# Kernel optimization log

Hardware: AMD Instinct MI355X
Metric: run time of the kernel (lower is better)

## Reference

```python
import math
import jax, jax.numpy as jnp
import numpy as np

L, F, K = 3, 128, 20          # layers, hidden size, rbf size
CUTOFF = 5.0
B, NPER, EPER = 4, 4096, 49152  # graphs, nodes/graph, edges/graph
NVOC = 119                    # len(ase.data.atomic_numbers)
PNAMES = ['atom_emb','pot_W','pot_b','init_W1','init_b1','init_W2','init_b2','vec_w',
          'filt_W','filt_b','msg_W1','msg_b1','msg_W2','msg_b2','U_W','V_W',
          'upd_W1','upd_b1','upd_W2','upd_b2']


def _painn(atom_xyz, cell, nodes, atom_edges, edges_displacement, V_flat, E_flat, p):
    N = B * NPER
    pos = atom_xyz.reshape(N, 3)
    # edge_offset = cumsum(num_nodes) ; all graphs have NPER nodes
    off = (jnp.arange(B, dtype=atom_edges.dtype) * NPER)[:, None, None]
    edges = (atom_edges + off).reshape(B * EPER, 2)
    # calc_distance with periodic cell offsets
    disp = jnp.einsum('bec,bcd->bed', edges_displacement, cell).reshape(B * EPER, 3)
    send, recv = edges[:, 0], edges[:, 1]
    diff = pos[recv] - (pos[send] + disp)                       # [E,3]
    dist = jnp.sqrt(jnp.sum(diff * diff, axis=1, keepdims=True))  # [E,1]
    # sinc RBF expansion
    n_range = jnp.arange(1, K + 1, dtype=jnp.float32)
    edge_state = jnp.sin(dist * n_range * (math.pi / CUTOFF)) / dist  # [E,K]
    # init scalar features: Embedding(Z) || Linear(V) -> MLP
    s_atom = p['atom_emb'][nodes.reshape(N)]                    # [N,F]
    s_pot = V_flat @ p['pot_W'].T + p['pot_b']                  # [N,F]
    h = jnp.concatenate([s_atom, s_pot], axis=-1)
    s = jax.nn.silu(h @ p['init_W1'].T + p['init_b1']) @ p['init_W2'].T + p['init_b2']  # [N,F]
    # init vector features: no-bias Linear(1->F) on E field
    v = E_flat[:, :, None] * p['vec_w']                         # [N,3,F]
    cut = jnp.where(dist < CUTOFF, 0.5 * (jnp.cos(math.pi * dist / CUTOFF) + 1.0), 0.0)  # [E,1]
    dirn = diff / jnp.maximum(dist, 1e-12)                      # [E,3]
    s_list, v_list = [], []
    for l in range(L):
        # --- PaiNNInteraction ---
        fw = (edge_state @ p['filt_W'][l].T + p['filt_b'][l]) * cut                # [E,3F]
        so = jax.nn.silu(s @ p['msg_W1'][l].T + p['msg_b1'][l]) @ p['msg_W2'][l].T + p['msg_b2'][l]  # [N,3F]
        fo = fw * so[send]                                                          # [E,3F]
        g_sv, g_ev, g_ns = jnp.split(fo, 3, axis=1)
        msg_s = s[send] * g_ns                                                      # [E,F]
        msg_v = v[send] * g_sv[:, None, :] + g_ev[:, None, :] * dirn[:, :, None]    # [E,3,F]
        s = s + jax.ops.segment_sum(msg_s, recv, num_segments=N)
        v = v + jax.ops.segment_sum(msg_v, recv, num_segments=N)
        # --- PaiNNUpdate ---
        Uv = v @ p['U_W'][l].T                                                      # [N,3,F]
        Vv = v @ p['V_W'][l].T                                                      # [N,3,F]
        Vn = jnp.sqrt(jnp.sum(Vv * Vv, axis=1))                                     # [N,F]
        m = jnp.concatenate([s, Vn], axis=1)
        m = jax.nn.silu(m @ p['upd_W1'][l].T + p['upd_b1'][l]) @ p['upd_W2'][l].T + p['upd_b2'][l]
        a_ss, a_sv, a_vv = jnp.split(m, 3, axis=1)
        s = s + a_ss + a_sv * jnp.sum(Uv * Vv, axis=1)
        v = v + a_vv[:, None, :] * Uv
        s_list.append(s)
        v_list.append(v)
    # pack trajectory: [L,N,1,F] scalar || [L,N,3,F] vector -> [L,N,4,F]
    return jnp.concatenate([jnp.stack(s_list)[:, :, None, :], jnp.stack(v_list)], axis=2)


def setup_inputs() -> dict:
    key = jax.random.key(0)
    ks = iter(jax.random.split(key, 48))
    def nrm(shape, scale=0.05):
        return jax.random.normal(next(ks), shape, dtype=jnp.float32) * scale
    atom_xyz = jax.random.uniform(next(ks), (B, NPER, 3), dtype=jnp.float32) * 30.0
    cell = jnp.tile(jnp.eye(3, dtype=jnp.float32)[None] * 30.0, (B, 1, 1))
    nodes = jax.random.randint(next(ks), (B, NPER), 0, NVOC)
    e0 = jax.random.randint(next(ks), (B, EPER), 0, NPER)
    delta = jax.random.randint(next(ks), (B, EPER), 1, NPER)
    e1 = (e0 + delta) % NPER  # sender != receiver -> no zero-distance edges
    atom_edges = jnp.stack([e0, e1], axis=-1)
    edges_displacement = jax.random.randint(next(ks), (B, EPER, 3), -1, 2).astype(jnp.float32)
    V_flat = nrm((B * NPER, 1), 1.0)
    E_flat = nrm((B * NPER, 3), 1.0)
    params = dict(
        atom_emb=nrm((NVOC, F), 1.0),
        pot_W=nrm((F, 1)), pot_b=nrm((F,)),
        init_W1=nrm((F, 2 * F)), init_b1=nrm((F,)),
        init_W2=nrm((F, F)), init_b2=nrm((F,)),
        vec_w=nrm((F,)),
        filt_W=nrm((L, 3 * F, K)), filt_b=nrm((L, 3 * F)),
        msg_W1=nrm((L, F, F)), msg_b1=nrm((L, F)),
        msg_W2=nrm((L, 3 * F, F)), msg_b2=nrm((L, 3 * F)),
        U_W=nrm((L, F, F)), V_W=nrm((L, F, F)),
        upd_W1=nrm((L, F, 2 * F)), upd_b1=nrm((L, F)),
        upd_W2=nrm((L, 3 * F, F)), upd_b2=nrm((L, 3 * F)),
    )
    return dict(atom_xyz=atom_xyz, cell=cell, nodes=nodes, atom_edges=atom_edges,
                edges_displacement=edges_displacement, V_flat=V_flat, E_flat=E_flat, **params)


def reference(atom_xyz, cell, nodes, atom_edges, edges_displacement, V_flat, E_flat,
              atom_emb, pot_W, pot_b, init_W1, init_b1, init_W2, init_b2, vec_w,
              filt_W, filt_b, msg_W1, msg_b1, msg_W2, msg_b2, U_W, V_W,
              upd_W1, upd_b1, upd_W2, upd_b2):
    p = dict(zip(PNAMES, (atom_emb, pot_W, pot_b, init_W1, init_b1, init_W2, init_b2, vec_w,
                          filt_W, filt_b, msg_W1, msg_b1, msg_W2, msg_b2, U_W, V_W,
                          upd_W1, upd_b1, upd_W2, upd_b2)))
    return _painn(atom_xyz, cell, nodes, atom_edges, edges_displacement, V_flat, E_flat, p)
```

## Files before the change

### kernel.cpp

```cpp
#include <hip/hip_runtime.h>
#include <math.h>

#define NPER  4096
#define NTOT  16384
#define EPER  49152
#define ETOT  196608
#define FD    128
#define F3    384
#define KR    20
#define PI_F  3.14159265358979f

typedef unsigned short u16;
typedef __attribute__((ext_vector_type(8))) short s16x8;
typedef __attribute__((ext_vector_type(4))) float f32x4;
typedef _Float16 h16x2 __attribute__((ext_vector_type(2)));
typedef _Float16 h16x4 __attribute__((ext_vector_type(4)));
typedef _Float16 h16x8 __attribute__((ext_vector_type(8)));

#if defined(__has_builtin)
#if __has_builtin(__builtin_amdgcn_fdot2)
#define FDOT2(a,b,c) __builtin_amdgcn_fdot2((a),(b),(c),false)
#endif
#endif
#ifndef FDOT2
#define FDOT2(a,b,c) ((float)(a)[0]*(float)(b)[0] + (float)(a)[1]*(float)(b)[1] + (c))
#endif

__device__ __forceinline__ float silu_f(float x){ return x / (1.0f + __expf(-x)); }
__device__ __forceinline__ u16 f2b(float x){
    unsigned u = __float_as_uint(x);
    u = u + 0x7FFFu + ((u >> 16) & 1u);
    return (u16)(u >> 16);
}
__device__ __forceinline__ float b2f(u16 h){ return __uint_as_float(((unsigned)h) << 16); }

struct __align__(16) EdgeRec {
    float4 ed;
    h16x8  es0;
    h16x8  es1;
    h16x4  es2;
    h16x4  pad;
};

__global__ __launch_bounds__(256) void edge_kernel(
    const float* __restrict__ xyz, const float* __restrict__ cell,
    const int* __restrict__ aedges, const float* __restrict__ edisp,
    int* __restrict__ sendb, int* __restrict__ recvb,
    EdgeRec* __restrict__ erec, int* __restrict__ counts)
{
    int e = blockIdx.x * blockDim.x + threadIdx.x;
    if (e >= ETOT) return;
    int b = e / EPER;
    int s = aedges[(size_t)e*2+0] + b*NPER;
    int r = aedges[(size_t)e*2+1] + b*NPER;
    const float* cb = cell + b*9;
    float c0 = edisp[(size_t)e*3+0], c1 = edisp[(size_t)e*3+1], c2 = edisp[(size_t)e*3+2];
    float diff[3];
    #pragma unroll
    for (int d=0; d<3; ++d) {
        float disp = c0*cb[d] + c1*cb[3+d] + c2*cb[6+d];
        diff[d] = xyz[(size_t)r*3+d] - (xyz[(size_t)s*3+d] + disp);
    }
    float dist = sqrtf(diff[0]*diff[0]+diff[1]*diff[1]+diff[2]*diff[2]);
    float cut = (dist < 5.0f) ? 0.5f*(__cosf(PI_F*dist*0.2f)+1.0f) : 0.0f;
    float invg = 1.0f/fmaxf(dist,1e-12f);
    EdgeRec rec;
    rec.ed = make_float4(diff[0]*invg, diff[1]*invg, diff[2]*invg, cut);
    float theta = dist*(PI_F*0.2f);
    float s1 = __sinf(theta), cth = __cosf(theta);
    float scale = cut / dist;
    float twoc = 2.f*cth;
    float sm1 = 0.f, sk = s1;
    _Float16 esv[20];
    #pragma unroll
    for (int k=0;k<20;++k){
        esv[k] = (_Float16)(sk*scale);
        float nx = twoc*sk - sm1;
        sm1 = sk; sk = nx;
    }
    union { h16x8 v; _Float16 h[8]; } u0, u1;
    union { h16x4 v; _Float16 h[4]; } u2;
    #pragma unroll
    for (int i=0;i<8;++i){ u0.h[i]=esv[i]; u1.h[i]=esv[8+i]; }
    #pragma unroll
    for (int i=0;i<4;++i) u2.h[i]=esv[16+i];
    rec.es0=u0.v; rec.es1=u1.v; rec.es2=u2.v;
    rec.pad = (h16x4)((_Float16)0);
    erec[e] = rec;
    sendb[e]=s; recvb[e]=r;
    atomicAdd(&counts[r],1);
}

__global__ __launch_bounds__(1024) void scan_kernel(const int* __restrict__ counts,
                                                    int* __restrict__ row_off)
{
    __shared__ int sdata[1024];
    int t = threadIdx.x;
    int base = t * 16;
    int local[16];
    int s = 0;
    #pragma unroll
    for (int i=0;i<16;++i){ local[i]=s; s += counts[base+i]; }
    sdata[t] = s;
    __syncthreads();
    for (int off=1; off<1024; off<<=1) {
        int val = (t>=off) ? sdata[t-off] : 0;
        __syncthreads();
        sdata[t] += val;
        __syncthreads();
    }
    int chunk_off = (t==0) ? 0 : sdata[t-1];
    #pragma unroll
    for (int i=0;i<16;++i) row_off[base+i] = chunk_off + local[i];
    if (t==1023) row_off[NTOT] = sdata[1023];
}

__global__ __launch_bounds__(256) void fill_kernel(
    const int* __restrict__ recvb, const int* __restrict__ sendb,
    const EdgeRec* __restrict__ erec,
    const int* __restrict__ row_off, int* __restrict__ cursor,
    int* __restrict__ sd_csr, EdgeRec* __restrict__ erec_csr)
{
    int e = blockIdx.x * blockDim.x + threadIdx.x;
    if (e >= ETOT) return;
    int r = recvb[e];
    int slot = atomicAdd(&cursor[r], 1);
    int pos = row_off[r] + slot;
    sd_csr[pos] = sendb[e];
    erec_csr[pos] = erec[e];
}

__global__ __launch_bounds__(256) void wconv_kernel(
    const float* __restrict__ w0, const float* __restrict__ w1,
    const float* __restrict__ w2, const float* __restrict__ w3,
    const float* __restrict__ w4, const float* __restrict__ w5,
    const float* __restrict__ w6, const float* __restrict__ w7,
    u16* __restrict__ dst)
{
    int t = blockIdx.x*256 + threadIdx.x;
    if (t >= 589824) return;
    const float* src; int off; int d = t;
    if      (t < 32768)  { src=w0; off=t; }
    else if (t < 49152)  { src=w1; off=t-32768; }
    else if (t < 98304)  { src=w2; off=t-49152; }
    else if (t < 245760) { src=w3; off=t-98304; }
    else if (t < 294912) { int o=t-245760; int l=o>>14; int r=o&16383; src=w4; off=o;
                           d = 245760 + l*32768 + r; }
    else if (t < 344064) { int o=t-294912; int l=o>>14; int r=o&16383; src=w5; off=o;
                           d = 245760 + l*32768 + 16384 + r; }
    else if (t < 442368) { src=w6; off=t-344064; }
    else                 { src=w7; off=t-442368; }
    dst[d] = f2b(src[off]);
}

__global__ __launch_bounds__(256) void wfilt_kernel(const float* __restrict__ fW,
                                                    _Float16* __restrict__ dst)
{
    int t = blockIdx.x*256 + threadIdx.x;
    if (t < 3*F3*KR) dst[t] = (_Float16)fW[t];
}

__global__ __launch_bounds__(256) void hbuild_kernel(const int* __restrict__ nodes,
    const float* __restrict__ atom_emb, const float* __restrict__ V_flat,
    const float* __restrict__ pot_W, const float* __restrict__ pot_b,
    u16* __restrict__ h)
{
    int t = blockIdx.x * blockDim.x + threadIdx.x;
    int n = t >> 8, k = t & 255;
    float val;
    if (k < FD) val = atom_emb[(size_t)nodes[n]*FD + k];
    else { int f = k - FD; val = V_flat[n]*pot_W[f] + pot_b[f]; }
    h[t] = f2b(val);
}

__global__ __launch_bounds__(256) void v0_kernel(const float* __restrict__ E_flat,
    const float* __restrict__ vec_w, float* __restrict__ v0, u16* __restrict__ vq)
{
    int t = blockIdx.x * blockDim.x + threadIdx.x;
    int n = t / F3, r = t - n*F3;
    int c = r >> 7, f = r & 127;
    float val = E_flat[(size_t)n*3 + c] * vec_w[f];
    v0[t] = val;
    vq[((size_t)n*FD + f)*4 + c] = f2b(val);
}

template<int ACT>
__global__ __launch_bounds__(256) void bgemm_kernel(
    const u16* __restrict__ A, int lda,
    const u16* __restrict__ W, int Kdim,
    const float* __restrict__ bias,
    float* __restrict__ C, int ldc,
    u16* __restrict__ Cb, int ldcb,
    u16* __restrict__ Cq, int qoff)
{
    const int tid  = threadIdx.x;
    const int wave = tid >> 6, lane = tid & 63;
    const int q = lane >> 4, im = lane & 15;
    const int row0 = blockIdx.y*64 + wave*16;
    const int col0 = blockIdx.x*64;
    f32x4 acc[4];
    #pragma unroll
    for (int n=0;n<4;++n) acc[n] = (f32x4){0.f,0.f,0.f,0.f};
    const u16* Ap = A + (size_t)(row0+im)*lda + q*8;
    const u16* Wp = W + (size_t)(col0+im)*Kdim + q*8;
    for (int k0 = 0; k0 < Kdim; k0 += 32) {
        s16x8 af = *(const s16x8*)(Ap + k0);
        #pragma unroll
        for (int n=0;n<4;++n) {
            s16x8 bf = *(const s16x8*)(Wp + (size_t)n*16*Kdim + k0);
            acc[n] = __builtin_amdgcn_mfma_f32_16x16x32_bf16(af, bf, acc[n], 0, 0, 0);
        }
    }
    #pragma unroll
    for (int n=0;n<4;++n) {
        int col = col0 + n*16 + im;
        float bv = bias ? bias[col] : 0.f;
        #pragma unroll
        for (int r=0;r<4;++r) {
            int row = row0 + q*4 + r;
            float v = acc[n][r] + bv;
            if (ACT) v = silu_f(v);
            if (C)  C[(size_t)row*ldc + col] = v;
            if (Cb) Cb[(size_t)row*ldcb + col] = f2b(v);
            if (Cq) Cq[((size_t)row*FD + (col & 127))*4 + (col >> 7) + qoff] = f2b(v);
        }
    }
}

__global__ __launch_bounds__(256) void uvdot_kernel(
    const u16* __restrict__ A,
    const u16* __restrict__ W,
    float* __restrict__ Uv,
    float* __restrict__ dotb,
    u16* __restrict__ mbuf)
{
    const int tid  = threadIdx.x;
    const int wave = tid >> 6, lane = tid & 63;
    const int q = lane >> 4, im = lane & 15;
    const int row0 = blockIdx.x*64 + wave*16;
    const int node = (row0 >> 2) + q;
    const u16* Ap = A + (size_t)(row0+im)*FD + q*8;
    s16x8 af[4];
    #pragma unroll
    for (int k=0;k<4;++k) af[k] = *(const s16x8*)(Ap + k*32);
    #pragma unroll
    for (int j=0;j<8;++j) {
        f32x4 aU = (f32x4){0.f,0.f,0.f,0.f};
        f32x4 aV = (f32x4){0.f,0.f,0.f,0.f};
        const u16* WpU = W + (size_t)(j*16+im)*FD + q*8;
        const u16* WpV = WpU + (size_t)128*FD;
        #pragma unroll
        for (int k=0;k<4;++k) {
            s16x8 bU = *(const s16x8*)(WpU + k*32);
            s16x8 bV = *(const s16x8*)(WpV + k*32);
            aU = __builtin_amdgcn_mfma_f32_16x16x32_bf16(af[k], bU, aU, 0, 0, 0);
            aV = __builtin_amdgcn_mfma_f32_16x16x32_bf16(af[k], bV, aV, 0, 0, 0);
        }
        int fcol = j*16 + im;
        float u0=aU[0], u1=aU[1], u2=aU[2];
        float w0=aV[0], w1=aV[1], w2=aV[2];
        dotb[(size_t)node*FD + fcol] = u0*w0 + u1*w1 + u2*w2;
        mbuf[(size_t)node*256 + FD + fcol] = f2b(sqrtf(w0*w0 + w1*w1 + w2*w2));
        size_t ub = ((size_t)node*4)*FD + fcol;
        Uv[ub]      = u0;
        Uv[ub+FD]   = u1;
        Uv[ub+2*FD] = u2;
    }
}

__global__ __launch_bounds__(256) void updepi_kernel(
    const u16* __restrict__ A,
    const u16* __restrict__ W,
    const float* __restrict__ bias,
    const float* __restrict__ s_mid, const float* __restrict__ dotb,
    const float* __restrict__ v_mid, const float* __restrict__ Uv,
    float* __restrict__ outp, u16* __restrict__ s_bf,
    u16* __restrict__ sq, u16* __restrict__ vq)
{
    const int tid  = threadIdx.x;
    const int wave = tid >> 6, lane = tid & 63;
    const int q = lane >> 4, im = lane & 15;
    const int rowgrp = wave >> 1, jhalf = wave & 1;
    const int row0 = blockIdx.x*32 + rowgrp*16;
    const u16* Ap = A + (size_t)(row0+im)*FD + q*8;

    for (int j = jhalf*4; j < jhalf*4+4; ++j) {
        f32x4 acc[3];
        #pragma unroll
        for (int g=0; g<3; ++g) acc[g] = (f32x4){0.f,0.f,0.f,0.f};
        const u16* Wp0 = W + (size_t)(j*16 + im)*FD + q*8;
        #pragma unroll
        for (int k0 = 0; k0 < FD; k0 += 32) {
            s16x8 af = *(const s16x8*)(Ap + k0);
            #pragma unroll
            for (int g=0; g<3; ++g) {
                s16x8 bf = *(const s16x8*)(Wp0 + (size_t)g*FD*FD + k0);
                acc[g] = __builtin_amdgcn_mfma_f32_16x16x32_bf16(af, bf, acc[g], 0, 0, 0);
            }
        }
        int fcol = j*16 + im;
        float b_ss = bias[fcol], b_sv = bias[FD+fcol], b_vv = bias[2*FD+fcol];
        #pragma unroll
        for (int r=0;r<4;++r) {
            int row = row0 + q*4 + r;
            float a_ss = acc[0][r] + b_ss;
            float a_sv = acc[1][r] + b_sv;
            float a_vv = acc[2][r] + b_vv;
            size_t t = (size_t)row*FD + fcol;
            float sval = s_mid[t] + a_ss + a_sv*dotb[t];
            outp[(size_t)row*512 + fcol] = sval;
            s_bf[t] = f2b(sval);
            sq[t*4 + 3] = f2b(sval);
            ushort4 pack;
            #pragma unroll
            for (int c=0;c<3;++c) {
                size_t vi = ((size_t)row*3 + c)*FD + fcol;
                float vval = v_mid[vi] + a_vv*Uv[((size_t)row*4 + c)*FD + fcol];
                outp[(size_t)row*512 + (1+c)*FD + fcol] = vval;
                ((u16*)&pack)[c] = f2b(vval);
            }
            ((u16*)&pack)[3] = 0;
            *(ushort4*)(vq + t*4) = pack;
        }
    }
}

__device__ __forceinline__ void edge_step(
    const EdgeRec& er, ushort4 s4, ushort4 v4,
    const h16x2* wp,
    float b0, float b1, float b2,
    float& acc_s, float& av0, float& av1, float& av2)
{
    union { h16x8 v; h16x2 p[4]; } e0, e1;
    union { h16x4 v; h16x2 p[2]; } e2;
    e0.v = er.es0; e1.v = er.es1; e2.v = er.es2;
    h16x2 ep[10] = {e0.p[0],e0.p[1],e0.p[2],e0.p[3],
                    e1.p[0],e1.p[1],e1.p[2],e1.p[3],
                    e2.p[0],e2.p[1]};
    float4 ed = er.ed;
    float d0=0.f, d1=0.f, d2=0.f;
    #pragma unroll
    for (int j=0;j<10;++j){
        d0 = FDOT2(ep[j], wp[j],    d0);
        d1 = FDOT2(ep[j], wp[10+j], d1);
        d2 = FDOT2(ep[j], wp[20+j], d2);
    }
    float g_sv = d0 + b0*ed.w;
    float g_ev = d1 + b1*ed.w;
    float g_ns = d2 + b2*ed.w;
    float fo_sv = g_sv * b2f(s4.x);
    float fo_ev = g_ev * b2f(s4.y);
    float fo_ns = g_ns * b2f(s4.z);
    acc_s += b2f(s4.w) * fo_ns;
    av0 += b2f(v4.x)*fo_sv + fo_ev*ed.x;
    av1 += b2f(v4.y)*fo_sv + fo_ev*ed.y;
    av2 += b2f(v4.z)*fo_sv + fo_ev*ed.z;
}

__global__ __launch_bounds__(256) __attribute__((amdgpu_waves_per_eu(4,8)))
void agg_kernel(
    const float* __restrict__ s_prev_f, int s_ldaf,
    const float* __restrict__ v_prev_f, int v_nstrf,
    const ushort4* __restrict__ sq, const ushort4* __restrict__ vq,
    const EdgeRec* __restrict__ erec_csr,
    const int* __restrict__ sd_csr, const int* __restrict__ row_off,
    const _Float16* __restrict__ wf, const float* __restrict__ fb,
    float* __restrict__ s_mid, float* __restrict__ v_mid,
    u16* __restrict__ vmid4_bf, u16* __restrict__ mbuf)
{
    const int f   = threadIdx.x & 127;
    const int sub = threadIdx.x >> 7;
    h16x2 wp[30];
    #pragma unroll
    for (int rsel=0; rsel<3; ++rsel){
        const h16x4* rp = (const h16x4*)(wf + (size_t)(rsel*FD + f)*KR);
        #pragma unroll
        for (int i=0;i<5;++i){
            union { h16x4 v; h16x2 p[2]; } t; t.v = rp[i];
            wp[rsel*10+2*i]   = t.p[0];
            wp[rsel*10+2*i+1] = t.p[1];
        }
    }
    const float b0 = fb[f], b1 = fb[FD+f], b2 = fb[2*FD+f];

    const int n = blockIdx.x*2 + sub;
    const int beg = __builtin_amdgcn_readfirstlane(row_off[n]);
    const int end = __builtin_amdgcn_readfirstlane(row_off[n+1]);
    float acc_s=0.f, av0=0.f, av1=0.f, av2=0.f;

    int i0 = (beg   < end) ? beg   : 0;
    int i1 = (beg+1 < end) ? beg+1 : i0;
    int sd0 = __builtin_amdgcn_readfirstlane(sd_csr[i0]);
    int sd1 = __builtin_amdgcn_readfirstlane(sd_csr[i1]);
    ushort4 sA = sq[(size_t)sd0*FD + f];
    ushort4 vA = vq[(size_t)sd0*FD + f];
    ushort4 sB = sq[(size_t)sd1*FD + f];
    ushort4 vB = vq[(size_t)sd1*FD + f];
    EdgeRec r0 = erec_csr[i0];
    EdgeRec r1 = erec_csr[i1];

    for (int idx = beg; idx + 2 <= end; idx += 2) {
        int j0 = (idx+2 < end) ? idx+2 : 0;
        int j1 = (idx+3 < end) ? idx+3 : j0;
        int nsd0 = __builtin_amdgcn_readfirstlane(sd_csr[j0]);
        int nsd1 = __builtin_amdgcn_readfirstlane(sd_csr[j1]);
        ushort4 nsA = sq[(size_t)nsd0*FD + f];
        ushort4 nvA = vq[(size_t)nsd0*FD + f];
        ushort4 nsB = sq[(size_t)nsd1*FD + f];
        ushort4 nvB = vq[(size_t)nsd1*FD + f];
        EdgeRec nr0 = erec_csr[j0];
        EdgeRec nr1 = erec_csr[j1];

        edge_step(r0, sA, vA, wp, b0,b1,b2, acc_s, av0, av1, av2);
        edge_step(r1, sB, vB, wp, b0,b1,b2, acc_s, av0, av1, av2);

        sA=nsA; vA=nvA; sB=nsB; vB=nvB; r0=nr0; r1=nr1;
    }
    if (((end - beg) & 1) && beg < end) {
        edge_step(r0, sA, vA, wp, b0,b1,b2, acc_s, av0, av1, av2);
    }

    float smv = s_prev_f[(size_t)n*s_ldaf+f] + acc_s;
    s_mid[(size_t)n*FD+f] = smv;
    mbuf[(size_t)n*256+f] = f2b(smv);
    const float* vp = v_prev_f + (size_t)n*v_nstrf;
    float o0 = vp[f]+av0, o1 = vp[FD+f]+av1, o2 = vp[2*FD+f]+av2;
    size_t vo = (size_t)n*F3;
    v_mid[vo+f]=o0;        v_mid[vo+FD+f]=o1;        v_mid[vo+2*FD+f]=o2;
    size_t v4 = (size_t)n*512;
    vmid4_bf[v4+f]=f2b(o0); vmid4_bf[v4+FD+f]=f2b(o1); vmid4_bf[v4+2*FD+f]=f2b(o2);
}

extern "C" void kernel_launch(void* const* d_in, const int* in_sizes, int n_in,
                              void* d_out, int out_size, void* d_ws, size_t ws_size,
                              hipStream_t stream)
{
    (void)in_sizes; (void)n_in; (void)out_size; (void)ws_size;
    const float* atom_xyz = (const float*)d_in[0];
    const float* cell     = (const float*)d_in[1];
    const int*   nodes    = (const int*)d_in[2];
    const int*   aedges   = (const int*)d_in[3];
    const float* edisp    = (const float*)d_in[4];
    const float* V_flat   = (const float*)d_in[5];
    const float* E_flat   = (const float*)d_in[6];
    const float* atom_emb = (const float*)d_in[7];
    const float* pot_W    = (const float*)d_in[8];
    const float* pot_b    = (const float*)d_in[9];
    const float* init_W1  = (const float*)d_in[10];
    const float* init_b1  = (const float*)d_in[11];
    const float* init_W2  = (const float*)d_in[12];
    const float* init_b2  = (const float*)d_in[13];
    const float* vec_w    = (const float*)d_in[14];
    const float* filt_W   = (const float*)d_in[15];
    const float* filt_b   = (const float*)d_in[16];
    const float* msg_W1   = (const float*)d_in[17];
    const float* msg_b1   = (const float*)d_in[18];
    const float* msg_W2   = (const float*)d_in[19];
    const float* msg_b2   = (const float*)d_in[20];
    const float* U_W      = (const float*)d_in[21];
    const float* V_W      = (const float*)d_in[22];
    const float* upd_W1   = (const float*)d_in[23];
    const float* upd_b1   = (const float*)d_in[24];
    const float* upd_W2   = (const float*)d_in[25];
    const float* upd_b2   = (const float*)d_in[26];

    float* out = (float*)d_out;
    char* base = (char*)d_ws;
    size_t o = 0;
    auto alloc = [&](size_t bytes)->char* { char* r = base + o; o += (bytes + 255) & ~(size_t)255; return r; };

    float* s0     = (float*)alloc((size_t)NTOT*FD*4);
    float* v0     = (float*)alloc((size_t)NTOT*F3*4);
    float* s_mid  = (float*)alloc((size_t)NTOT*FD*4);
    float* v_mid  = (float*)alloc((size_t)NTOT*F3*4);
    float* Uv4    = (float*)alloc((size_t)NTOT*4*FD*4);
    float* dotb   = (float*)alloc((size_t)NTOT*FD*4);
    EdgeRec* erec     = (EdgeRec*)alloc((size_t)ETOT*sizeof(EdgeRec));
    EdgeRec* erec_csr = (EdgeRec*)alloc((size_t)ETOT*sizeof(EdgeRec));
    u16* h_bf     = (u16*)alloc((size_t)NTOT*256*2);
    u16* s_bf     = (u16*)alloc((size_t)NTOT*FD*2);
    u16* sq       = (u16*)alloc((size_t)NTOT*FD*4*2);
    u16* vq       = (u16*)alloc((size_t)NTOT*FD*4*2);
    u16* hid_bf   = (u16*)alloc((size_t)NTOT*FD*2);
    u16* vmid4_bf = (u16*)alloc((size_t)NTOT*4*FD*2);
    u16* wts      = (u16*)alloc((size_t)589824*2);
    _Float16* wf16 = (_Float16*)alloc((size_t)3*F3*KR*2);
    int* sendb    = (int*)alloc((size_t)ETOT*4);
    int* recvb    = (int*)alloc((size_t)ETOT*4);
    int* sd_csr   = (int*)alloc((size_t)ETOT*4);
    int* row_off  = (int*)alloc((size_t)(NTOT+1)*4);
    int* counts   = (int*)alloc((size_t)NTOT*4);
    int* cursor   = (int*)alloc((size_t)NTOT*4);

    hipMemsetAsync(counts, 0, NTOT*sizeof(int), stream);
    hipMemsetAsync(cursor, 0, NTOT*sizeof(int), stream);
    hipMemsetAsync(vmid4_bf, 0, (size_t)NTOT*4*FD*2, stream);

    edge_kernel<<<ETOT/256, 256, 0, stream>>>(atom_xyz, cell, aedges, edisp,
        sendb, recvb, erec, counts);
    scan_kernel<<<1, 1024, 0, stream>>>(counts, row_off);
    fill_kernel<<<ETOT/256, 256, 0, stream>>>(recvb, sendb, erec,
        row_off, cursor, sd_csr, erec_csr);
    wconv_kernel<<<(589824+255)/256, 256, 0, stream>>>(
        init_W1, init_W2, msg_W1, msg_W2, U_W, V_W, upd_W1, upd_W2, wts);
    wfilt_kernel<<<(3*F3*KR+255)/256, 256, 0, stream>>>(filt_W, wf16);

    const u16* w_init1 = wts + 0;
    const u16* w_init2 = wts + 32768;
    const u16* w_msg1  = wts + 49152;
    const u16* w_msg2  = wts + 98304;
    const u16* w_UV    = wts + 245760;
    const u16* w_upd1  = wts + 344064;
    const u16* w_upd2  = wts + 442368;

    hbuild_kernel<<<NTOT*256/256, 256, 0, stream>>>(nodes, atom_emb, V_flat, pot_W, pot_b, h_bf);
    bgemm_kernel<1><<<dim3(FD/64, NTOT/64), 256, 0, stream>>>(
        h_bf, 256, w_init1, 256, init_b1, (float*)nullptr, 0, hid_bf, FD, (u16*)nullptr, 0);
    bgemm_kernel<0><<<dim3(FD/64, NTOT/64), 256, 0, stream>>>(
        hid_bf, FD, w_init2, FD, init_b2, s0, FD, s_bf, FD, sq, 3);
    v0_kernel<<<NTOT*F3/256, 256, 0, stream>>>(E_flat, vec_w, v0, vq);

    const float* s_prev_f = s0;  int s_ldaf  = FD;
    const float* v_prev_f = v0;  int v_nstrf = 3*FD;
    for (int l = 0; l < 3; ++l) {
        bgemm_kernel<1><<<dim3(FD/64, NTOT/64), 256, 0, stream>>>(
            s_bf, FD, w_msg1 + (size_t)l*16384, FD, msg_b1 + (size_t)l*FD,
            (float*)nullptr, 0, hid_bf, FD, (u16*)nullptr, 0);
        bgemm_kernel<0><<<dim3(F3/64, NTOT/64), 256, 0, stream>>>(
            hid_bf, FD, w_msg2 + (size_t)l*49152, FD, msg_b2 + (size_t)l*F3,
            (float*)nullptr, 0, (u16*)nullptr, 0, sq, 0);
        agg_kernel<<<NTOT/2, 256, 0, stream>>>(s_prev_f, s_ldaf, v_prev_f, v_nstrf,
            (const ushort4*)sq, (const ushort4*)vq, erec_csr, sd_csr, row_off,
            wf16 + (size_t)l*F3*KR, filt_b + (size_t)l*F3, s_mid, v_mid, vmid4_bf, h_bf);
        uvdot_kernel<<<NTOT*4/64, 256, 0, stream>>>(
            vmid4_bf, w_UV + (size_t)l*32768, Uv4, dotb, h_bf);
        bgemm_kernel<1><<<dim3(FD/64, NTOT/64), 256, 0, stream>>>(
            h_bf, 256, w_upd1 + (size_t)l*32768, 256, upd_b1 + (size_t)l*FD,
            (float*)nullptr, 0, hid_bf, FD, (u16*)nullptr, 0);
        float* outp = out + (size_t)l*NTOT*512;
        updepi_kernel<<<NTOT/32, 256, 0, stream>>>(
            hid_bf, w_upd2 + (size_t)l*49152, upd_b2 + (size_t)l*F3,
            s_mid, dotb, v_mid, Uv4, outp, s_bf, sq, vq);
        s_prev_f = outp;        s_ldaf  = 512;
        v_prev_f = outp + FD;   v_nstrf = 512;
    }
}
```

Baseline: 795.6 us.

## Fuse two-layer message and update MLPs into single kernels via LDS hidden tile

Replaces the pair of bgemm launches for the message MLP, and the bgemm plus updepi launches for the update MLP, with single 512-thread kernels. Each kernel computes the first GEMM with SiLU into an XOR-swizzled shared-memory hidden tile, then runs the second GEMM from LDS. This removes the hid_bf global round-trip and two launches per layer. In exchange, blocks are larger, LDS use per block is higher, and weights are read directly from global per wave, which may lower occupancy.

```diff
diff --git a/kernel.cpp b/kernel.cpp
--- a/kernel.cpp
+++ b/kernel.cpp
@@ -227,85 +227,156 @@
     }
 }
 
-__global__ __launch_bounds__(256) void uvdot_kernel(
+#define HID_OFF(row, col2b) ((unsigned)((row)*256 + (col2b)*2) ^ ((unsigned)((row)&7) << 4))
+
+__global__ __launch_bounds__(512) void msgmlp_kernel(
     const u16* __restrict__ A,
-    const u16* __restrict__ W,
-    float* __restrict__ Uv,
-    float* __restrict__ dotb,
-    u16* __restrict__ mbuf)
-{
-    const int tid  = threadIdx.x;
+    const u16* __restrict__ W1,
+    const float* __restrict__ b1,
+    const u16* __restrict__ W2,
+    const float* __restrict__ b2,
+    u16* __restrict__ sq)
+{
+    __shared__ u16 hid[64*FD];
+    const int tid = threadIdx.x;
     const int wave = tid >> 6, lane = tid & 63;
     const int q = lane >> 4, im = lane & 15;
-    const int row0 = blockIdx.x*64 + wave*16;
-    const int node = (row0 >> 2) + q;
-    const u16* Ap = A + (size_t)(row0+im)*FD + q*8;
+    const int rw = (wave >> 1) * 16;
+    const int ch = wave & 1;
+    const int row0 = blockIdx.x * 64;
+    {
+        f32x4 acc[4];
+        #pragma unroll
+        for (int n=0;n<4;++n) acc[n] = (f32x4){0.f,0.f,0.f,0.f};
+        const u16* Ap = A + (size_t)(row0+rw+im)*FD + q*8;
+        #pragma unroll
+        for (int k0=0;k0<FD;k0+=32) {
+            s16x8 af = *(const s16x8*)(Ap + k0);
+            #pragma unroll
+            for (int n=0;n<4;++n) {
+                s16x8 bf = *(const s16x8*)(W1 + (size_t)(ch*64+n*16+im)*FD + k0 + q*8);
+                acc[n] = __builtin_amdgcn_mfma_f32_16x16x32_bf16(af, bf, acc[n], 0, 0, 0);
+            }
+        }
+        #pragma unroll
+        for (int n=0;n<4;++n) {
+            int col = ch*64 + n*16 + im;
+            float bv = b1[col];
+            #pragma unroll
+            for (int r=0;r<4;++r) {
+                int row = rw + q*4 + r;
+                *(u16*)((char*)hid + HID_OFF(row, col)) = f2b(silu_f(acc[n][r]+bv));
+            }
+        }
+    }
+    __syncthreads();
     s16x8 af[4];
-    #pragma unroll
-    for (int k=0;k<4;++k) af[k] = *(const s16x8*)(Ap + k*32);
-    #pragma unroll
-    for (int j=0;j<8;++j) {
-        f32x4 aU = (f32x4){0.f,0.f,0.f,0.f};
-        f32x4 aV = (f32x4){0.f,0.f,0.f,0.f};
-        const u16* WpU = W + (size_t)(j*16+im)*FD + q*8;
-        const u16* WpV = WpU + (size_t)128*FD;
+    {
+        int row = rw + im;
+        #pragma unroll
+        for (int k=0;k<4;++k)
+            af[k] = *(const s16x8*)((char*)hid + HID_OFF(row, k*32+q*8));
+    }
+    #pragma unroll
+    for (int jj=0;jj<4;++jj) {
+        int j = ch*4 + jj;
+        f32x4 a2[3];
+        #pragma unroll
+        for (int g=0;g<3;++g) a2[g] = (f32x4){0.f,0.f,0.f,0.f};
         #pragma unroll
         for (int k=0;k<4;++k) {
-            s16x8 bU = *(const s16x8*)(WpU + k*32);
-            s16x8 bV = *(const s16x8*)(WpV + k*32);
-            aU = __builtin_amdgcn_mfma_f32_16x16x32_bf16(af[k], bU, aU, 0, 0, 0);
-            aV = __builtin_amdgcn_mfma_f32_16x16x32_bf16(af[k], bV, aV, 0, 0, 0);
+            #pragma unroll
+            for (int g=0;g<3;++g) {
+                s16x8 bf = *(const s16x8*)(W2 + (size_t)(g*128 + j*16 + im)*FD + k*32 + q*8);
+                a2[g] = __builtin_amdgcn_mfma_f32_16x16x32_bf16(af[k], bf, a2[g], 0, 0, 0);
+            }
         }
         int fcol = j*16 + im;
-        float u0=aU[0], u1=aU[1], u2=aU[2];
-        float w0=aV[0], w1=aV[1], w2=aV[2];
-        dotb[(size_t)node*FD + fcol] = u0*w0 + u1*w1 + u2*w2;
-        mbuf[(size_t)node*256 + FD + fcol] = f2b(sqrtf(w0*w0 + w1*w1 + w2*w2));
-        size_t ub = ((size_t)node*4)*FD + fcol;
-        Uv[ub]      = u0;
-        Uv[ub+FD]   = u1;
-        Uv[ub+2*FD] = u2;
-    }
-}
-
-__global__ __launch_bounds__(256) void updepi_kernel(
+        float c0 = b2[fcol], c1 = b2[FD+fcol], c2 = b2[2*FD+fcol];
+        #pragma unroll
+        for (int r=0;r<4;++r) {
+            int row = row0 + rw + q*4 + r;
+            size_t t4 = ((size_t)row*FD + fcol)*4;
+            unsigned pk = (unsigned)f2b(a2[0][r]+c0) | ((unsigned)f2b(a2[1][r]+c1) << 16);
+            *(unsigned*)(sq + t4) = pk;
+            sq[t4+2] = f2b(a2[2][r]+c2);
+        }
+    }
+}
+
+__global__ __launch_bounds__(512) void updmlp_kernel(
     const u16* __restrict__ A,
-    const u16* __restrict__ W,
-    const float* __restrict__ bias,
+    const u16* __restrict__ W1,
+    const float* __restrict__ b1,
+    const u16* __restrict__ W2,
+    const float* __restrict__ b2,
     const float* __restrict__ s_mid, const float* __restrict__ dotb,
     const float* __restrict__ v_mid, const float* __restrict__ Uv,
     float* __restrict__ outp, u16* __restrict__ s_bf,
     u16* __restrict__ sq, u16* __restrict__ vq)
 {
-    const int tid  = threadIdx.x;
+    __shared__ u16 hid[64*FD];
+    const int tid = threadIdx.x;
     const int wave = tid >> 6, lane = tid & 63;
     const int q = lane >> 4, im = lane & 15;
-    const int rowgrp = wave >> 1, jhalf = wave & 1;
-    const int row0 = blockIdx.x*32 + rowgrp*16;
-    const u16* Ap = A + (size_t)(row0+im)*FD + q*8;
-
-    for (int j = jhalf*4; j < jhalf*4+4; ++j) {
-        f32x4 acc[3];
-        #pragma unroll
-        for (int g=0; g<3; ++g) acc[g] = (f32x4){0.f,0.f,0.f,0.f};
-        const u16* Wp0 = W + (size_t)(j*16 + im)*FD + q*8;
-        #pragma unroll
-        for (int k0 = 0; k0 < FD; k0 += 32) {
+    const int rw = (wave >> 1) * 16;
+    const int ch = wave & 1;
+    const int row0 = blockIdx.x * 64;
+    {
+        f32x4 acc[4];
+        #pragma unroll
+        for (int n=0;n<4;++n) acc[n] = (f32x4){0.f,0.f,0.f,0.f};
+        const u16* Ap = A + (size_t)(row0+rw+im)*256 + q*8;
+        #pragma unroll
+        for (int k0=0;k0<256;k0+=32) {
             s16x8 af = *(const s16x8*)(Ap + k0);
             #pragma unroll
-            for (int g=0; g<3; ++g) {
-                s16x8 bf = *(const s16x8*)(Wp0 + (size_t)g*FD*FD + k0);
-                acc[g] = __builtin_amdgcn_mfma_f32_16x16x32_bf16(af, bf, acc[g], 0, 0, 0);
+            for (int n=0;n<4;++n) {
+                s16x8 bf = *(const s16x8*)(W1 + (size_t)(ch*64+n*16+im)*256 + k0 + q*8);
+                acc[n] = __builtin_amdgcn_mfma_f32_16x16x32_bf16(af, bf, acc[n], 0, 0, 0);
             }
         }
+        #pragma unroll
+        for (int n=0;n<4;++n) {
+            int col = ch*64 + n*16 + im;
+            float bv = b1[col];
+            #pragma unroll
+            for (int r=0;r<4;++r) {
+                int row = rw + q*4 + r;
+                *(u16*)((char*)hid + HID_OFF(row, col)) = f2b(silu_f(acc[n][r]+bv));
+            }
+        }
+    }
+    __syncthreads();
+    s16x8 af[4];
+    {
+        int row = rw + im;
+        #pragma unroll
+        for (int k=0;k<4;++k)
+            af[k] = *(const s16x8*)((char*)hid + HID_OFF(row, k*32+q*8));
+    }
+    #pragma unroll
+    for (int jj=0;jj<4;++jj) {
+        int j = ch*4 + jj;
+        f32x4 a2[3];
+        #pragma unroll
+        for (int g=0;g<3;++g) a2[g] = (f32x4){0.f,0.f,0.f,0.f};
+        #pragma unroll
+        for (int k=0;k<4;++k) {
+            #pragma unroll
+            for (int g=0;g<3;++g) {
+                s16x8 bf = *(const s16x8*)(W2 + (size_t)(g*128 + j*16 + im)*FD + k*32 + q*8);
+                a2[g] = __builtin_amdgcn_mfma_f32_16x16x32_bf16(af[k], bf, a2[g], 0, 0, 0);
+            }
+        }
         int fcol = j*16 + im;
-        float b_ss = bias[fcol], b_sv = bias[FD+fcol], b_vv = bias[2*FD+fcol];
+        float b_ss = b2[fcol], b_sv = b2[FD+fcol], b_vv = b2[2*FD+fcol];
         #pragma unroll
         for (int r=0;r<4;++r) {
-            int row = row0 + q*4 + r;
-            float a_ss = acc[0][r] + b_ss;
-            float a_sv = acc[1][r] + b_sv;
-            float a_vv = acc[2][r] + b_vv;
+            int row = row0 + rw + q*4 + r;
+            float a_ss = a2[0][r] + b_ss;
+            float a_sv = a2[1][r] + b_sv;
+            float a_vv = a2[2][r] + b_vv;
             size_t t = (size_t)row*FD + fcol;
             float sval = s_mid[t] + a_ss + a_sv*dotb[t];
             outp[(size_t)row*512 + fcol] = sval;
@@ -322,6 +393,47 @@
             ((u16*)&pack)[3] = 0;
             *(ushort4*)(vq + t*4) = pack;
         }
+    }
+}
+
+__global__ __launch_bounds__(256) void uvdot_kernel(
+    const u16* __restrict__ A,
+    const u16* __restrict__ W,
+    float* __restrict__ Uv,
+    float* __restrict__ dotb,
+    u16* __restrict__ mbuf)
+{
+    const int tid  = threadIdx.x;
+    const int wave = tid >> 6, lane = tid & 63;
+    const int q = lane >> 4, im = lane & 15;
+    const int row0 = blockIdx.x*64 + wave*16;
+    const int node = (row0 >> 2) + q;
+    const u16* Ap = A + (size_t)(row0+im)*FD + q*8;
+    s16x8 af[4];
+    #pragma unroll
+    for (int k=0;k<4;++k) af[k] = *(const s16x8*)(Ap + k*32);
+    #pragma unroll
+    for (int j=0;j<8;++j) {
+        f32x4 aU = (f32x4){0.f,0.f,0.f,0.f};
+        f32x4 aV = (f32x4){0.f,0.f,0.f,0.f};
+        const u16* WpU = W + (size_t)(j*16+im)*FD + q*8;
+        const u16* WpV = WpU + (size_t)128*FD;
+        #pragma unroll
+        for (int k=0;k<4;++k) {
+            s16x8 bU = *(const s16x8*)(WpU + k*32);
+            s16x8 bV = *(const s16x8*)(WpV + k*32);
+            aU = __builtin_amdgcn_mfma_f32_16x16x32_bf16(af[k], bU, aU, 0, 0, 0);
+            aV = __builtin_amdgcn_mfma_f32_16x16x32_bf16(af[k], bV, aV, 0, 0, 0);
+        }
+        int fcol = j*16 + im;
+        float u0=aU[0], u1=aU[1], u2=aU[2];
+        float w0=aV[0], w1=aV[1], w2=aV[2];
+        dotb[(size_t)node*FD + fcol] = u0*w0 + u1*w1 + u2*w2;
+        mbuf[(size_t)node*256 + FD + fcol] = f2b(sqrtf(w0*w0 + w1*w1 + w2*w2));
+        size_t ub = ((size_t)node*4)*FD + fcol;
+        Uv[ub]      = u0;
+        Uv[ub+FD]   = u1;
+        Uv[ub+2*FD] = u2;
     }
 }
 
@@ -523,23 +635,18 @@
     const float* s_prev_f = s0;  int s_ldaf  = FD;
     const float* v_prev_f = v0;  int v_nstrf = 3*FD;
     for (int l = 0; l < 3; ++l) {
-        bgemm_kernel<1><<<dim3(FD/64, NTOT/64), 256, 0, stream>>>(
-            s_bf, FD, w_msg1 + (size_t)l*16384, FD, msg_b1 + (size_t)l*FD,
-            (float*)nullptr, 0, hid_bf, FD, (u16*)nullptr, 0);
-        bgemm_kernel<0><<<dim3(F3/64, NTOT/64), 256, 0, stream>>>(
-            hid_bf, FD, w_msg2 + (size_t)l*49152, FD, msg_b2 + (size_t)l*F3,
-            (float*)nullptr, 0, (u16*)nullptr, 0, sq, 0);
+        msgmlp_kernel<<<NTOT/64, 512, 0, stream>>>(
+            s_bf, w_msg1 + (size_t)l*16384, msg_b1 + (size_t)l*FD,
+            w_msg2 + (size_t)l*49152, msg_b2 + (size_t)l*F3, sq);
         agg_kernel<<<NTOT/2, 256, 0, stream>>>(s_prev_f, s_ldaf, v_prev_f, v_nstrf,
             (const ushort4*)sq, (const ushort4*)vq, erec_csr, sd_csr, row_off,
             wf16 + (size_t)l*F3*KR, filt_b + (size_t)l*F3, s_mid, v_mid, vmid4_bf, h_bf);
         uvdot_kernel<<<NTOT*4/64, 256, 0, stream>>>(
             vmid4_bf, w_UV + (size_t)l*32768, Uv4, dotb, h_bf);
-        bgemm_kernel<1><<<dim3(FD/64, NTOT/64), 256, 0, stream>>>(
-            h_bf, 256, w_upd1 + (size_t)l*32768, 256, upd_b1 + (size_t)l*FD,
-            (float*)nullptr, 0, hid_bf, FD, (u16*)nullptr, 0);
         float* outp = out + (size_t)l*NTOT*512;
-        updepi_kernel<<<NTOT/32, 256, 0, stream>>>(
-            hid_bf, w_upd2 + (size_t)l*49152, upd_b2 + (size_t)l*F3,
+        updmlp_kernel<<<NTOT/64, 512, 0, stream>>>(
+            h_bf, w_upd1 + (size_t)l*32768, upd_b1 + (size_t)l*FD,
+            w_upd2 + (size_t)l*49152, upd_b2 + (size_t)l*F3,
             s_mid, dotb, v_mid, Uv4, outp, s_bf, sq, vq);
         s_prev_f = outp;        s_ldaf  = 512;
         v_prev_f = outp + FD;   v_nstrf = 512;
```

Measured after the change: 769.6 us. 1.03x faster.
